# Kernel optimization log

Measured on AMD Instinct MI355X. Metric: run time of the kernel, lower is better.

Reference implementation:

```python
import jax, jax.numpy as jnp
import numpy as np

B, N, M = 262144, 8, 4  # batch, state dim, measurement dim


def _tril_square(x, n):
    """x: (b, n(n+1)/2) linearized lower-tri elems -> L @ L.T, (b, n, n)."""
    i, j = np.tril_indices(n)
    L = jnp.zeros((x.shape[0], n, n), dtype=x.dtype).at[:, i, j].set(x)
    return jnp.einsum('bik,bjk->bij', L, L)


def setup_inputs() -> dict:
    key = jax.random.key(0)
    ks = jax.random.split(key, 7)
    measurement = jax.random.normal(ks[0], (B, M), dtype=jnp.float32)
    state = jax.random.normal(ks[1], (B, N), dtype=jnp.float32)
    # SPD state covariance: A A^T / n + I
    A = jax.random.normal(ks[2], (B, N, N), dtype=jnp.float32) * 0.3
    state_cov = jnp.einsum('bik,bjk->bij', A, A) / N + jnp.eye(N, dtype=jnp.float32)
    F = jnp.eye(N, dtype=jnp.float32) + 0.1 * jax.random.normal(ks[3], (B, N, N), dtype=jnp.float32)
    H = jax.random.normal(ks[4], (B, M, N), dtype=jnp.float32) * 0.5
    process_noise = jax.random.normal(ks[5], (B, N * (N + 1) // 2), dtype=jnp.float32) * 0.1
    measurement_noise = jax.random.normal(ks[6], (B, M * (M + 1) // 2), dtype=jnp.float32) * 0.3
    return {
        'measurement': measurement, 'state': state, 'state_cov': state_cov,
        'F': F, 'H': H,
        'process_noise': process_noise, 'measurement_noise': measurement_noise,
    }


def reference(measurement, state, state_cov, F, H, process_noise, measurement_noise):
    b, n = state.shape
    m = measurement.shape[1]
    Q = _tril_square(process_noise, n)       # (b, n, n) process noise cov
    R = _tril_square(measurement_noise, m)   # (b, m, m) measurement noise cov

    # Predict
    new_state = jnp.einsum('bij,bj->bi', F, state)
    new_state_cov = jnp.einsum('bij,bjk,blk->bil', F, state_cov, F) + Q

    # Update
    prediction = jnp.einsum('bij,bj->bi', H, new_state)
    res = measurement - prediction
    res_cov = jnp.einsum('bij,bjk,blk->bil', H, new_state_cov, H) + R  # (b, m, m)
    PHt = jnp.einsum('bij,bkj->bik', new_state_cov, H)                 # (b, n, m)
    kgain = jnp.matmul(PHt, jnp.linalg.inv(res_cov))                   # (b, n, m)

    upd_state = new_state + jnp.einsum('bij,bj->bi', kgain, res)
    I = jnp.eye(n, dtype=state.dtype)
    upd_cov = jnp.matmul(I - jnp.matmul(kgain, H), new_state_cov)
    return prediction, upd_state, upd_cov
```

## Files before the change

### kernel.cpp

```cpp
#include <hip/hip_runtime.h>

#define DEVINL __device__ __forceinline__

#define TIX(i, j) ((i) * ((i) + 1) / 2 + (j))
#define SYM(arr, i, j) ((i) >= (j) ? arr[TIX(i, j)] : arr[TIX(j, i)])

DEVINL void inv4(const float* m, float* inv) {
    float s0 = m[0] * m[5] - m[1] * m[4];
    float s1 = m[0] * m[6] - m[2] * m[4];
    float s2 = m[0] * m[7] - m[3] * m[4];
    float s3 = m[1] * m[6] - m[2] * m[5];
    float s4 = m[1] * m[7] - m[3] * m[5];
    float s5 = m[2] * m[7] - m[3] * m[6];
    float c5 = m[10] * m[15] - m[11] * m[14];
    float c4 = m[9] * m[15] - m[11] * m[13];
    float c3 = m[9] * m[14] - m[10] * m[13];
    float c2 = m[8] * m[15] - m[11] * m[12];
    float c1 = m[8] * m[14] - m[10] * m[12];
    float c0 = m[8] * m[13] - m[9] * m[12];
    float det = s0 * c5 - s1 * c4 + s2 * c3 + s3 * c2 - s4 * c1 + s5 * c0;
    float id = 1.0f / det;
    inv[0]  = ( m[5] * c5 - m[6] * c4 + m[7] * c3) * id;
    inv[1]  = (-m[1] * c5 + m[2] * c4 - m[3] * c3) * id;
    inv[2]  = ( m[13] * s5 - m[14] * s4 + m[15] * s3) * id;
    inv[3]  = (-m[9] * s5 + m[10] * s4 - m[11] * s3) * id;
    inv[4]  = (-m[4] * c5 + m[6] * c2 - m[7] * c1) * id;
    inv[5]  = ( m[0] * c5 - m[2] * c2 + m[3] * c1) * id;
    inv[6]  = (-m[12] * s5 + m[14] * s2 - m[15] * s1) * id;
    inv[7]  = ( m[8] * s5 - m[10] * s2 + m[11] * s1) * id;
    inv[8]  = ( m[4] * c4 - m[5] * c2 + m[7] * c0) * id;
    inv[9]  = (-m[0] * c4 + m[1] * c2 - m[3] * c0) * id;
    inv[10] = ( m[12] * s4 - m[13] * s2 + m[15] * s0) * id;
    inv[11] = (-m[8] * s4 + m[9] * s2 - m[11] * s0) * id;
    inv[12] = (-m[4] * c3 + m[5] * c1 - m[6] * c0) * id;
    inv[13] = ( m[0] * c3 - m[1] * c1 + m[2] * c0) * id;
    inv[14] = (-m[12] * s3 + m[13] * s1 - m[14] * s0) * id;
    inv[15] = ( m[8] * s3 - m[9] * s1 + m[10] * s0) * id;
}

__global__ __launch_bounds__(256) void ekf_kernel(
    const float* __restrict__ meas,
    const float* __restrict__ state,
    const float* __restrict__ Pin,
    const float* __restrict__ Fin,
    const float* __restrict__ Hin,
    const float* __restrict__ pnin,
    const float* __restrict__ mnin,
    float* __restrict__ out_pred,
    float* __restrict__ out_state,
    float* __restrict__ out_cov,
    int B)
{
    const int b = blockIdx.x * blockDim.x + threadIdx.x;
    if (b >= B) return;

    float Pn[36];
    {
        float Lq[36];
        const float4* p4 = reinterpret_cast<const float4*>(pnin + (size_t)b * 36);
        #pragma unroll
        for (int i = 0; i < 9; ++i) {
            float4 v = p4[i];
            Lq[4 * i] = v.x; Lq[4 * i + 1] = v.y; Lq[4 * i + 2] = v.z; Lq[4 * i + 3] = v.w;
        }
        #pragma unroll
        for (int i = 0; i < 8; ++i)
            #pragma unroll
            for (int j = 0; j <= i; ++j) {
                float acc = 0.f;
                #pragma unroll
                for (int k = 0; k <= j; ++k)
                    acc += Lq[TIX(i, k)] * Lq[TIX(j, k)];
                Pn[TIX(i, j)] = acc;
            }
    }

    float Fm[64];
    {
        const float4* f4 = reinterpret_cast<const float4*>(Fin + (size_t)b * 64);
        #pragma unroll
        for (int i = 0; i < 16; ++i) {
            float4 v = f4[i];
            Fm[4 * i] = v.x; Fm[4 * i + 1] = v.y; Fm[4 * i + 2] = v.z; Fm[4 * i + 3] = v.w;
        }
    }
    float Ps[36];
    {
        const float4* p4 = reinterpret_cast<const float4*>(Pin + (size_t)b * 64);
        #pragma unroll
        for (int i = 0; i < 16; ++i) {
            float4 v = p4[i];
            const int row = i / 2, c0 = (i % 2) * 4;
            if (c0 + 0 <= row) Ps[TIX(row, c0 + 0)] = v.x;
            if (c0 + 1 <= row) Ps[TIX(row, c0 + 1)] = v.y;
            if (c0 + 2 <= row) Ps[TIX(row, c0 + 2)] = v.z;
            if (c0 + 3 <= row) Ps[TIX(row, c0 + 3)] = v.w;
        }
    }
    float s[8];
    {
        const float4* s4 = reinterpret_cast<const float4*>(state + (size_t)b * 8);
        float4 a = s4[0], c = s4[1];
        s[0] = a.x; s[1] = a.y; s[2] = a.z; s[3] = a.w;
        s[4] = c.x; s[5] = c.y; s[6] = c.z; s[7] = c.w;
    }

    float ns[8];
    #pragma unroll
    for (int i = 0; i < 8; ++i) {
        float acc = 0.f;
        #pragma unroll
        for (int j = 0; j < 8; ++j) acc += Fm[i * 8 + j] * s[j];
        ns[i] = acc;
    }

    {
        float T[64];
        #pragma unroll
        for (int i = 0; i < 8; ++i)
            #pragma unroll
            for (int k = 0; k < 8; ++k) {
                float acc = 0.f;
                #pragma unroll
                for (int j = 0; j < 8; ++j) acc += Fm[i * 8 + j] * SYM(Ps, j, k);
                T[i * 8 + k] = acc;
            }
        #pragma unroll
        for (int i = 0; i < 8; ++i)
            #pragma unroll
            for (int l = 0; l <= i; ++l) {
                float acc = Pn[TIX(i, l)];
                #pragma unroll
                for (int k = 0; k < 8; ++k) acc += T[i * 8 + k] * Fm[l * 8 + k];
                Pn[TIX(i, l)] = acc;
            }
    }

    float Hm[32];
    {
        const float4* h4 = reinterpret_cast<const float4*>(Hin + (size_t)b * 32);
        #pragma unroll
        for (int i = 0; i < 8; ++i) {
            float4 v = h4[i];
            Hm[4 * i] = v.x; Hm[4 * i + 1] = v.y; Hm[4 * i + 2] = v.z; Hm[4 * i + 3] = v.w;
        }
    }
    float Rs[10];
    {
        float Lr[10];
        const float2* m2 = reinterpret_cast<const float2*>(mnin + (size_t)b * 10);
        #pragma unroll
        for (int i = 0; i < 5; ++i) {
            float2 v = m2[i];
            Lr[2 * i] = v.x; Lr[2 * i + 1] = v.y;
        }
        #pragma unroll
        for (int i = 0; i < 4; ++i)
            #pragma unroll
            for (int j = 0; j <= i; ++j) {
                float acc = 0.f;
                #pragma unroll
                for (int k = 0; k <= j; ++k)
                    acc += Lr[TIX(i, k)] * Lr[TIX(j, k)];
                Rs[TIX(i, j)] = acc;
            }
    }

    float pred[4], res[4];
    {
        float4 z = *reinterpret_cast<const float4*>(meas + (size_t)b * 4);
        const float zz[4] = {z.x, z.y, z.z, z.w};
        #pragma unroll
        for (int i = 0; i < 4; ++i) {
            float acc = 0.f;
            #pragma unroll
            for (int j = 0; j < 8; ++j) acc += Hm[i * 8 + j] * ns[j];
            pred[i] = acc;
            res[i] = zz[i] - acc;
        }
    }

    float HP[32];
    #pragma unroll
    for (int i = 0; i < 4; ++i)
        #pragma unroll
        for (int k = 0; k < 8; ++k) {
            float acc = 0.f;
            #pragma unroll
            for (int j = 0; j < 8; ++j) acc += Hm[i * 8 + j] * SYM(Pn, j, k);
            HP[i * 8 + k] = acc;
        }

    float Si[16];
    {
        float Sf[16];
        #pragma unroll
        for (int i = 0; i < 4; ++i)
            #pragma unroll
            for (int l = 0; l < 4; ++l) {
                float acc = SYM(Rs, i, l);
                #pragma unroll
                for (int k = 0; k < 8; ++k) acc += HP[i * 8 + k] * Hm[l * 8 + k];
                Sf[i * 4 + l] = acc;
            }
        inv4(Sf, Si);
    }

    float K[32];
    #pragma unroll
    for (int i = 0; i < 8; ++i)
        #pragma unroll
        for (int j = 0; j < 4; ++j) {
            float acc = 0.f;
            #pragma unroll
            for (int k = 0; k < 4; ++k) acc += HP[k * 8 + i] * Si[k * 4 + j];
            K[i * 4 + j] = acc;
        }

    float* op = out_pred + (size_t)b * 4;
    *reinterpret_cast<float4*>(op) = make_float4(pred[0], pred[1], pred[2], pred[3]);

    float us[8];
    #pragma unroll
    for (int i = 0; i < 8; ++i) {
        float acc = ns[i];
        #pragma unroll
        for (int j = 0; j < 4; ++j) acc += K[i * 4 + j] * res[j];
        us[i] = acc;
    }
    float* osp = out_state + (size_t)b * 8;
    *reinterpret_cast<float4*>(osp + 0) = make_float4(us[0], us[1], us[2], us[3]);
    *reinterpret_cast<float4*>(osp + 4) = make_float4(us[4], us[5], us[6], us[7]);

    float* ocp = out_cov + (size_t)b * 64;
    #pragma unroll
    for (int i = 0; i < 8; ++i) {
        float Arow[8];
        #pragma unroll
        for (int j = 0; j < 8; ++j) {
            float acc = (i == j) ? 1.f : 0.f;
            #pragma unroll
            for (int k = 0; k < 4; ++k) acc -= K[i * 4 + k] * Hm[k * 8 + j];
            Arow[j] = acc;
        }
        float orow[8];
        #pragma unroll
        for (int j = 0; j < 8; ++j) {
            float acc = 0.f;
            #pragma unroll
            for (int k = 0; k < 8; ++k) acc += Arow[k] * SYM(Pn, k, j);
            orow[j] = acc;
        }
        *reinterpret_cast<float4*>(ocp + i * 8 + 0) = make_float4(orow[0], orow[1], orow[2], orow[3]);
        *reinterpret_cast<float4*>(ocp + i * 8 + 4) = make_float4(orow[4], orow[5], orow[6], orow[7]);
    }
}

extern "C" void kernel_launch(void* const* d_in, const int* in_sizes, int n_in,
                              void* d_out, int out_size, void* d_ws, size_t ws_size,
                              hipStream_t stream) {
    const float* meas  = (const float*)d_in[0];
    const float* state = (const float*)d_in[1];
    const float* Pin   = (const float*)d_in[2];
    const float* Fin   = (const float*)d_in[3];
    const float* Hin   = (const float*)d_in[4];
    const float* pn    = (const float*)d_in[5];
    const float* mn    = (const float*)d_in[6];

    const int B = in_sizes[1] / 8;

    float* out = (float*)d_out;
    float* out_pred  = out;
    float* out_state = out + (size_t)B * 4;
    float* out_cov   = out + (size_t)B * 12;

    dim3 block(256);
    dim3 grid((B + 255) / 256);
    ekf_kernel<<<grid, block, 0, stream>>>(meas, state, Pin, Fin, Hin, pn, mn,
                                           out_pred, out_state, out_cov, B);
}
```

Before: 271.6 us.

## Stage per-batch loads and stores through padded shared memory for coalescing

Each block now cooperatively loads the per-element inputs (process noise, state, covariance, F, H, measurement noise) into a padded shared buffer with contiguous float4 accesses, then each thread reads its own rows from LDS. The covariance and state outputs are written back the same way. This replaces strided per-thread global float4 accesses (64-256 byte stride) with coalesced ones. It also restructures F·P·F^T into column-wise products, avoiding the 64-entry temporary, and adds a minimum-occupancy launch bound. The cost is many block-wide barriers, about 36 KB of shared memory per block, and extra register pressure under the occupancy hint.

```diff
diff --git a/kernel.cpp b/kernel.cpp
--- a/kernel.cpp
+++ b/kernel.cpp
@@ -38,7 +38,7 @@
     inv[15] = ( m[8] * s3 - m[9] * s1 + m[10] * s0) * id;
 }
 
-__global__ __launch_bounds__(256) void ekf_kernel(
+__global__ __launch_bounds__(256, 3) void ekf_kernel(
     const float* __restrict__ meas,
     const float* __restrict__ state,
     const float* __restrict__ Pin,
@@ -51,17 +51,28 @@
     float* __restrict__ out_cov,
     int B)
 {
-    const int b = blockIdx.x * blockDim.x + threadIdx.x;
-    if (b >= B) return;
-
+    const int t  = threadIdx.x;
+    const int bb = blockIdx.x * 256;
+    const int nb = min(256, B - bb);
+    const int b  = bb + t;
+    const bool act = (t < nb);
+
+    __shared__ float4 buf[2304];
+
+    {
+        const float4* g = reinterpret_cast<const float4*>(pnin) + (size_t)bb * 9;
+        const int lim = nb * 9;
+        #pragma unroll
+        for (int i = 0; i < 9; ++i) { int f = i * 256 + t; if (f < lim) buf[f] = g[f]; }
+    }
+    __syncthreads();
     float Pn[36];
-    {
+    if (act) {
         float Lq[36];
-        const float4* p4 = reinterpret_cast<const float4*>(pnin + (size_t)b * 36);
-        #pragma unroll
-        for (int i = 0; i < 9; ++i) {
-            float4 v = p4[i];
-            Lq[4 * i] = v.x; Lq[4 * i + 1] = v.y; Lq[4 * i + 2] = v.z; Lq[4 * i + 3] = v.w;
+        #pragma unroll
+        for (int q = 0; q < 9; ++q) {
+            float4 v = buf[t * 9 + q];
+            Lq[4 * q] = v.x; Lq[4 * q + 1] = v.y; Lq[4 * q + 2] = v.z; Lq[4 * q + 3] = v.w;
         }
         #pragma unroll
         for (int i = 0; i < 8; ++i)
@@ -74,85 +85,145 @@
                 Pn[TIX(i, j)] = acc;
             }
     }
-
-    float Fm[64];
-    {
-        const float4* f4 = reinterpret_cast<const float4*>(Fin + (size_t)b * 64);
-        #pragma unroll
-        for (int i = 0; i < 16; ++i) {
-            float4 v = f4[i];
-            Fm[4 * i] = v.x; Fm[4 * i + 1] = v.y; Fm[4 * i + 2] = v.z; Fm[4 * i + 3] = v.w;
-        }
-    }
-    float Ps[36];
-    {
-        const float4* p4 = reinterpret_cast<const float4*>(Pin + (size_t)b * 64);
-        #pragma unroll
-        for (int i = 0; i < 16; ++i) {
-            float4 v = p4[i];
-            const int row = i / 2, c0 = (i % 2) * 4;
-            if (c0 + 0 <= row) Ps[TIX(row, c0 + 0)] = v.x;
-            if (c0 + 1 <= row) Ps[TIX(row, c0 + 1)] = v.y;
-            if (c0 + 2 <= row) Ps[TIX(row, c0 + 2)] = v.z;
-            if (c0 + 3 <= row) Ps[TIX(row, c0 + 3)] = v.w;
-        }
-    }
+    __syncthreads();
+
+    {
+        const float4* g = reinterpret_cast<const float4*>(state) + (size_t)bb * 2;
+        const int lim = nb * 2;
+        #pragma unroll
+        for (int i = 0; i < 2; ++i) {
+            int f = i * 256 + t;
+            if (f < lim) buf[(f >> 1) * 3 + (f & 1)] = g[f];
+        }
+    }
+    __syncthreads();
     float s[8];
-    {
-        const float4* s4 = reinterpret_cast<const float4*>(state + (size_t)b * 8);
-        float4 a = s4[0], c = s4[1];
+    if (act) {
+        float4 a = buf[t * 3 + 0], c = buf[t * 3 + 1];
         s[0] = a.x; s[1] = a.y; s[2] = a.z; s[3] = a.w;
         s[4] = c.x; s[5] = c.y; s[6] = c.z; s[7] = c.w;
     }
+    __syncthreads();
+
+    float Ps[36];
+    #pragma unroll
+    for (int h = 0; h < 2; ++h) {
+        {
+            const float4* g = reinterpret_cast<const float4*>(Pin) + (size_t)bb * 16;
+            #pragma unroll
+            for (int i = 0; i < 8; ++i) {
+                int fl = i * 256 + t;
+                int bq = fl >> 3, q = fl & 7;
+                if (bq < nb) buf[bq * 9 + q] = g[bq * 16 + 8 * h + q];
+            }
+        }
+        __syncthreads();
+        if (act) {
+            #pragma unroll
+            for (int q = 0; q < 8; ++q) {
+                float4 v = buf[t * 9 + q];
+                const int row = 4 * h + (q >> 1), c0 = 4 * (q & 1);
+                if (c0 + 0 <= row) Ps[TIX(row, c0 + 0)] = v.x;
+                if (c0 + 1 <= row) Ps[TIX(row, c0 + 1)] = v.y;
+                if (c0 + 2 <= row) Ps[TIX(row, c0 + 2)] = v.z;
+                if (c0 + 3 <= row) Ps[TIX(row, c0 + 3)] = v.w;
+            }
+        }
+        __syncthreads();
+    }
+
+    float Fm[64];
+    #pragma unroll
+    for (int h = 0; h < 2; ++h) {
+        {
+            const float4* g = reinterpret_cast<const float4*>(Fin) + (size_t)bb * 16;
+            #pragma unroll
+            for (int i = 0; i < 8; ++i) {
+                int fl = i * 256 + t;
+                int bq = fl >> 3, q = fl & 7;
+                if (bq < nb) buf[bq * 9 + q] = g[bq * 16 + 8 * h + q];
+            }
+        }
+        __syncthreads();
+        if (act) {
+            #pragma unroll
+            for (int q = 0; q < 8; ++q) {
+                float4 v = buf[t * 9 + q];
+                Fm[32 * h + 4 * q + 0] = v.x;
+                Fm[32 * h + 4 * q + 1] = v.y;
+                Fm[32 * h + 4 * q + 2] = v.z;
+                Fm[32 * h + 4 * q + 3] = v.w;
+            }
+        }
+        __syncthreads();
+    }
 
     float ns[8];
-    #pragma unroll
-    for (int i = 0; i < 8; ++i) {
-        float acc = 0.f;
-        #pragma unroll
-        for (int j = 0; j < 8; ++j) acc += Fm[i * 8 + j] * s[j];
-        ns[i] = acc;
-    }
-
-    {
-        float T[64];
-        #pragma unroll
-        for (int i = 0; i < 8; ++i)
-            #pragma unroll
-            for (int k = 0; k < 8; ++k) {
-                float acc = 0.f;
-                #pragma unroll
-                for (int j = 0; j < 8; ++j) acc += Fm[i * 8 + j] * SYM(Ps, j, k);
-                T[i * 8 + k] = acc;
-            }
-        #pragma unroll
-        for (int i = 0; i < 8; ++i)
-            #pragma unroll
-            for (int l = 0; l <= i; ++l) {
+    if (act) {
+        #pragma unroll
+        for (int i = 0; i < 8; ++i) {
+            float acc = 0.f;
+            #pragma unroll
+            for (int j = 0; j < 8; ++j) acc += Fm[i * 8 + j] * s[j];
+            ns[i] = acc;
+        }
+        #pragma unroll
+        for (int l = 0; l < 8; ++l) {
+            float gcol[8];
+            #pragma unroll
+            for (int j = 0; j < 8; ++j) {
+                float acc = 0.f;
+                #pragma unroll
+                for (int k = 0; k < 8; ++k) acc += SYM(Ps, j, k) * Fm[l * 8 + k];
+                gcol[j] = acc;
+            }
+            #pragma unroll
+            for (int i = l; i < 8; ++i) {
                 float acc = Pn[TIX(i, l)];
                 #pragma unroll
-                for (int k = 0; k < 8; ++k) acc += T[i * 8 + k] * Fm[l * 8 + k];
+                for (int j = 0; j < 8; ++j) acc += Fm[i * 8 + j] * gcol[j];
                 Pn[TIX(i, l)] = acc;
             }
+        }
     }
 
     float Hm[32];
     {
-        const float4* h4 = reinterpret_cast<const float4*>(Hin + (size_t)b * 32);
+        const float4* g = reinterpret_cast<const float4*>(Hin) + (size_t)bb * 8;
+        const int lim = nb * 8;
         #pragma unroll
         for (int i = 0; i < 8; ++i) {
-            float4 v = h4[i];
-            Hm[4 * i] = v.x; Hm[4 * i + 1] = v.y; Hm[4 * i + 2] = v.z; Hm[4 * i + 3] = v.w;
-        }
-    }
+            int fl = i * 256 + t;
+            if (fl < lim) buf[(fl >> 3) * 9 + (fl & 7)] = g[fl];
+        }
+    }
+    __syncthreads();
+    if (act) {
+        #pragma unroll
+        for (int q = 0; q < 8; ++q) {
+            float4 v = buf[t * 9 + q];
+            Hm[4 * q + 0] = v.x; Hm[4 * q + 1] = v.y;
+            Hm[4 * q + 2] = v.z; Hm[4 * q + 3] = v.w;
+        }
+    }
+    __syncthreads();
+
     float Rs[10];
     {
+        const float2* g = reinterpret_cast<const float2*>(mnin) + (size_t)bb * 5;
+        float2* buf2 = reinterpret_cast<float2*>(buf);
+        const int lim = nb * 5;
+        #pragma unroll
+        for (int i = 0; i < 5; ++i) { int f = i * 256 + t; if (f < lim) buf2[f] = g[f]; }
+    }
+    __syncthreads();
+    if (act) {
+        const float2* buf2 = reinterpret_cast<const float2*>(buf);
         float Lr[10];
-        const float2* m2 = reinterpret_cast<const float2*>(mnin + (size_t)b * 10);
-        #pragma unroll
-        for (int i = 0; i < 5; ++i) {
-            float2 v = m2[i];
-            Lr[2 * i] = v.x; Lr[2 * i + 1] = v.y;
+        #pragma unroll
+        for (int p = 0; p < 5; ++p) {
+            float2 v = buf2[t * 5 + p];
+            Lr[2 * p] = v.x; Lr[2 * p + 1] = v.y;
         }
         #pragma unroll
         for (int i = 0; i < 4; ++i)
@@ -165,10 +236,11 @@
                 Rs[TIX(i, j)] = acc;
             }
     }
-
-    float pred[4], res[4];
-    {
-        float4 z = *reinterpret_cast<const float4*>(meas + (size_t)b * 4);
+    __syncthreads();
+
+    float pred[4], res[4], HP[32], Si[16], K[32], us[8];
+    if (act) {
+        float4 z = *(reinterpret_cast<const float4*>(meas) + b);
         const float zz[4] = {z.x, z.y, z.z, z.w};
         #pragma unroll
         for (int i = 0; i < 4; ++i) {
@@ -178,21 +250,17 @@
             pred[i] = acc;
             res[i] = zz[i] - acc;
         }
-    }
-
-    float HP[32];
-    #pragma unroll
-    for (int i = 0; i < 4; ++i)
-        #pragma unroll
-        for (int k = 0; k < 8; ++k) {
-            float acc = 0.f;
-            #pragma unroll
-            for (int j = 0; j < 8; ++j) acc += Hm[i * 8 + j] * SYM(Pn, j, k);
-            HP[i * 8 + k] = acc;
-        }
-
-    float Si[16];
-    {
+
+        #pragma unroll
+        for (int i = 0; i < 4; ++i)
+            #pragma unroll
+            for (int k = 0; k < 8; ++k) {
+                float acc = 0.f;
+                #pragma unroll
+                for (int j = 0; j < 8; ++j) acc += Hm[i * 8 + j] * SYM(Pn, j, k);
+                HP[i * 8 + k] = acc;
+            }
+
         float Sf[16];
         #pragma unroll
         for (int i = 0; i < 4; ++i)
@@ -204,55 +272,83 @@
                 Sf[i * 4 + l] = acc;
             }
         inv4(Sf, Si);
-    }
-
-    float K[32];
+
+        #pragma unroll
+        for (int i = 0; i < 8; ++i)
+            #pragma unroll
+            for (int j = 0; j < 4; ++j) {
+                float acc = 0.f;
+                #pragma unroll
+                for (int k = 0; k < 4; ++k) acc += HP[k * 8 + i] * Si[k * 4 + j];
+                K[i * 4 + j] = acc;
+            }
+
+        *(reinterpret_cast<float4*>(out_pred) + b) =
+            make_float4(pred[0], pred[1], pred[2], pred[3]);
+
+        #pragma unroll
+        for (int i = 0; i < 8; ++i) {
+            float acc = ns[i];
+            #pragma unroll
+            for (int j = 0; j < 4; ++j) acc += K[i * 4 + j] * res[j];
+            us[i] = acc;
+        }
+    }
+
+    __syncthreads();
+    if (act) {
+        buf[t * 3 + 0] = make_float4(us[0], us[1], us[2], us[3]);
+        buf[t * 3 + 1] = make_float4(us[4], us[5], us[6], us[7]);
+    }
+    __syncthreads();
+    {
+        float4* g = reinterpret_cast<float4*>(out_state) + (size_t)bb * 2;
+        const int lim = nb * 2;
+        #pragma unroll
+        for (int i = 0; i < 2; ++i) {
+            int f = i * 256 + t;
+            if (f < lim) g[f] = buf[(f >> 1) * 3 + (f & 1)];
+        }
+    }
+    __syncthreads();
+
     #pragma unroll
-    for (int i = 0; i < 8; ++i)
-        #pragma unroll
-        for (int j = 0; j < 4; ++j) {
-            float acc = 0.f;
-            #pragma unroll
-            for (int k = 0; k < 4; ++k) acc += HP[k * 8 + i] * Si[k * 4 + j];
-            K[i * 4 + j] = acc;
-        }
-
-    float* op = out_pred + (size_t)b * 4;
-    *reinterpret_cast<float4*>(op) = make_float4(pred[0], pred[1], pred[2], pred[3]);
-
-    float us[8];
-    #pragma unroll
-    for (int i = 0; i < 8; ++i) {
-        float acc = ns[i];
-        #pragma unroll
-        for (int j = 0; j < 4; ++j) acc += K[i * 4 + j] * res[j];
-        us[i] = acc;
-    }
-    float* osp = out_state + (size_t)b * 8;
-    *reinterpret_cast<float4*>(osp + 0) = make_float4(us[0], us[1], us[2], us[3]);
-    *reinterpret_cast<float4*>(osp + 4) = make_float4(us[4], us[5], us[6], us[7]);
-
-    float* ocp = out_cov + (size_t)b * 64;
-    #pragma unroll
-    for (int i = 0; i < 8; ++i) {
-        float Arow[8];
-        #pragma unroll
-        for (int j = 0; j < 8; ++j) {
-            float acc = (i == j) ? 1.f : 0.f;
-            #pragma unroll
-            for (int k = 0; k < 4; ++k) acc -= K[i * 4 + k] * Hm[k * 8 + j];
-            Arow[j] = acc;
-        }
-        float orow[8];
-        #pragma unroll
-        for (int j = 0; j < 8; ++j) {
-            float acc = 0.f;
-            #pragma unroll
-            for (int k = 0; k < 8; ++k) acc += Arow[k] * SYM(Pn, k, j);
-            orow[j] = acc;
-        }
-        *reinterpret_cast<float4*>(ocp + i * 8 + 0) = make_float4(orow[0], orow[1], orow[2], orow[3]);
-        *reinterpret_cast<float4*>(ocp + i * 8 + 4) = make_float4(orow[4], orow[5], orow[6], orow[7]);
+    for (int h = 0; h < 2; ++h) {
+        if (act) {
+            #pragma unroll
+            for (int r = 0; r < 4; ++r) {
+                const int i = 4 * h + r;
+                float Arow[8];
+                #pragma unroll
+                for (int j = 0; j < 8; ++j) {
+                    float acc = (i == j) ? 1.f : 0.f;
+                    #pragma unroll
+                    for (int k = 0; k < 4; ++k) acc -= K[i * 4 + k] * Hm[k * 8 + j];
+                    Arow[j] = acc;
+                }
+                float orow[8];
+                #pragma unroll
+                for (int j = 0; j < 8; ++j) {
+                    float acc = 0.f;
+                    #pragma unroll
+                    for (int k = 0; k < 8; ++k) acc += Arow[k] * SYM(Pn, k, j);
+                    orow[j] = acc;
+                }
+                buf[t * 9 + 2 * r + 0] = make_float4(orow[0], orow[1], orow[2], orow[3]);
+                buf[t * 9 + 2 * r + 1] = make_float4(orow[4], orow[5], orow[6], orow[7]);
+            }
+        }
+        __syncthreads();
+        {
+            float4* g = reinterpret_cast<float4*>(out_cov) + (size_t)bb * 16;
+            #pragma unroll
+            for (int i = 0; i < 8; ++i) {
+                int fl = i * 256 + t;
+                int bq = fl >> 3, q = fl & 7;
+                if (bq < nb) g[bq * 16 + 8 * h + q] = buf[bq * 9 + q];
+            }
+        }
+        __syncthreads();
     }
 }
 
```

New measurement: 342.1 us. 1.26x slower.

## Split each Kalman filter batch across 8 lanes with shuffle-based row math

Applied to the files above, without the earlier changes.

Instead of one thread per batch element holding full 8x8 matrices in registers, each batch element is now handled by 8 lanes, one per state row. Matrix products and reductions are exchanged via width-8 shuffles. The covariance update is rewritten as P - (HP)^T S^-1 (HP), dropping the explicit Kalman gain and the I-KH product. The aim is to cut register pressure, raise occupancy and coalesce loads and stores. In exchange, the 4x4 inverse is computed redundantly in every lane, and the bounds check is dropped, so B*8 must be a multiple of 256.

```diff
diff --git a/kernel.cpp b/kernel.cpp
--- a/kernel.cpp
+++ b/kernel.cpp
@@ -1,9 +1,7 @@
 #include <hip/hip_runtime.h>
 
 #define DEVINL __device__ __forceinline__
-
 #define TIX(i, j) ((i) * ((i) + 1) / 2 + (j))
-#define SYM(arr, i, j) ((i) >= (j) ? arr[TIX(i, j)] : arr[TIX(j, i)])
 
 DEVINL void inv4(const float* m, float* inv) {
     float s0 = m[0] * m[5] - m[1] * m[4];
@@ -48,212 +46,153 @@
     const float* __restrict__ mnin,
     float* __restrict__ out_pred,
     float* __restrict__ out_state,
-    float* __restrict__ out_cov,
-    int B)
+    float* __restrict__ out_cov)
 {
-    const int b = blockIdx.x * blockDim.x + threadIdx.x;
-    if (b >= B) return;
-
-    float Pn[36];
+    const int gt = blockIdx.x * 256 + threadIdx.x;
+    const int b  = gt >> 3;
+    const int r  = gt & 7;
+
+    float fr[8], pr[8];
     {
-        float Lq[36];
-        const float4* p4 = reinterpret_cast<const float4*>(pnin + (size_t)b * 36);
-        #pragma unroll
-        for (int i = 0; i < 9; ++i) {
-            float4 v = p4[i];
-            Lq[4 * i] = v.x; Lq[4 * i + 1] = v.y; Lq[4 * i + 2] = v.z; Lq[4 * i + 3] = v.w;
-        }
-        #pragma unroll
-        for (int i = 0; i < 8; ++i)
+        const float4* gf = reinterpret_cast<const float4*>(Fin + (size_t)b * 64 + r * 8);
+        float4 a = gf[0], c = gf[1];
+        fr[0]=a.x; fr[1]=a.y; fr[2]=a.z; fr[3]=a.w;
+        fr[4]=c.x; fr[5]=c.y; fr[6]=c.z; fr[7]=c.w;
+        const float4* gp = reinterpret_cast<const float4*>(Pin + (size_t)b * 64 + r * 8);
+        float4 d = gp[0], e = gp[1];
+        pr[0]=d.x; pr[1]=d.y; pr[2]=d.z; pr[3]=d.w;
+        pr[4]=e.x; pr[5]=e.y; pr[6]=e.z; pr[7]=e.w;
+    }
+    float lq[8];
+    {
+        const float* lp = pnin + (size_t)b * 36 + ((r * (r + 1)) >> 1);
+        #pragma unroll
+        for (int k = 0; k < 8; ++k) { float v = lp[k]; lq[k] = (k <= r) ? v : 0.f; }
+    }
+    float hc[4];
+    #pragma unroll
+    for (int a = 0; a < 4; ++a) hc[a] = Hin[(size_t)b * 32 + a * 8 + r];
+    float sc = state[(size_t)b * 8 + r];
+    float4 z = *reinterpret_cast<const float4*>(meas + (size_t)b * 4);
+
+    float ns = 0.f;
+    #pragma unroll
+    for (int j = 0; j < 8; ++j) ns += fr[j] * __shfl(sc, j, 8);
+
+    float g[8];
+    #pragma unroll
+    for (int l = 0; l < 8; ++l) {
+        float acc = 0.f;
+        #pragma unroll
+        for (int k = 0; k < 8; ++k) acc += pr[k] * __shfl(fr[k], l, 8);
+        g[l] = acc;
+    }
+
+    float pn_[8] = {0, 0, 0, 0, 0, 0, 0, 0};
+    #pragma unroll
+    for (int j = 0; j < 8; ++j) {
+        const float frj = fr[j];
+        #pragma unroll
+        for (int l = 0; l < 8; ++l) pn_[l] += frj * __shfl(g[l], j, 8);
+    }
+
+    #pragma unroll
+    for (int l = 0; l < 8; ++l) {
+        float acc = 0.f;
+        #pragma unroll
+        for (int k = 0; k <= l; ++k) acc += lq[k] * __shfl(lq[k], l, 8);
+        pn_[l] += acc;
+    }
+
+    float pd[4];
+    #pragma unroll
+    for (int a = 0; a < 4; ++a) pd[a] = hc[a] * ns;
+    #pragma unroll
+    for (int a = 0; a < 4; ++a) {
+        pd[a] += __shfl_xor(pd[a], 1, 8);
+        pd[a] += __shfl_xor(pd[a], 2, 8);
+        pd[a] += __shfl_xor(pd[a], 4, 8);
+    }
+    float res[4] = { z.x - pd[0], z.y - pd[1], z.z - pd[2], z.w - pd[3] };
+    if (r < 4) {
+        float pv = pd[0];
+        pv = (r == 1) ? pd[1] : pv;
+        pv = (r == 2) ? pd[2] : pv;
+        pv = (r == 3) ? pd[3] : pv;
+        out_pred[(size_t)b * 4 + r] = pv;
+    }
+
+    float hp[4] = {0, 0, 0, 0};
+    #pragma unroll
+    for (int j = 0; j < 8; ++j) {
+        const float pj = pn_[j];
+        #pragma unroll
+        for (int a = 0; a < 4; ++a) hp[a] += pj * __shfl(hc[a], j, 8);
+    }
+
+    float S[16];
+    #pragma unroll
+    for (int a = 0; a < 4; ++a)
+        #pragma unroll
+        for (int c = 0; c < 4; ++c) S[a * 4 + c] = hp[a] * hc[c];
+    #pragma unroll
+    for (int e = 0; e < 16; ++e) {
+        S[e] += __shfl_xor(S[e], 1, 8);
+        S[e] += __shfl_xor(S[e], 2, 8);
+        S[e] += __shfl_xor(S[e], 4, 8);
+    }
+    {
+        float lr[10];
+        const float2* g2 = reinterpret_cast<const float2*>(mnin + (size_t)b * 10);
+        #pragma unroll
+        for (int i = 0; i < 5; ++i) { float2 v = g2[i]; lr[2 * i] = v.x; lr[2 * i + 1] = v.y; }
+        #pragma unroll
+        for (int a = 0; a < 4; ++a)
             #pragma unroll
-            for (int j = 0; j <= i; ++j) {
+            for (int c = 0; c <= a; ++c) {
                 float acc = 0.f;
                 #pragma unroll
-                for (int k = 0; k <= j; ++k)
-                    acc += Lq[TIX(i, k)] * Lq[TIX(j, k)];
-                Pn[TIX(i, j)] = acc;
+                for (int k = 0; k <= c; ++k) acc += lr[TIX(a, k)] * lr[TIX(c, k)];
+                S[a * 4 + c] += acc;
+                if (a != c) S[c * 4 + a] += acc;
             }
     }
-
-    float Fm[64];
-    {
-        const float4* f4 = reinterpret_cast<const float4*>(Fin + (size_t)b * 64);
-        #pragma unroll
-        for (int i = 0; i < 16; ++i) {
-            float4 v = f4[i];
-            Fm[4 * i] = v.x; Fm[4 * i + 1] = v.y; Fm[4 * i + 2] = v.z; Fm[4 * i + 3] = v.w;
-        }
-    }
-    float Ps[36];
-    {
-        const float4* p4 = reinterpret_cast<const float4*>(Pin + (size_t)b * 64);
-        #pragma unroll
-        for (int i = 0; i < 16; ++i) {
-            float4 v = p4[i];
-            const int row = i / 2, c0 = (i % 2) * 4;
-            if (c0 + 0 <= row) Ps[TIX(row, c0 + 0)] = v.x;
-            if (c0 + 1 <= row) Ps[TIX(row, c0 + 1)] = v.y;
-            if (c0 + 2 <= row) Ps[TIX(row, c0 + 2)] = v.z;
-            if (c0 + 3 <= row) Ps[TIX(row, c0 + 3)] = v.w;
-        }
-    }
-    float s[8];
-    {
-        const float4* s4 = reinterpret_cast<const float4*>(state + (size_t)b * 8);
-        float4 a = s4[0], c = s4[1];
-        s[0] = a.x; s[1] = a.y; s[2] = a.z; s[3] = a.w;
-        s[4] = c.x; s[5] = c.y; s[6] = c.z; s[7] = c.w;
-    }
-
-    float ns[8];
-    #pragma unroll
-    for (int i = 0; i < 8; ++i) {
-        float acc = 0.f;
-        #pragma unroll
-        for (int j = 0; j < 8; ++j) acc += Fm[i * 8 + j] * s[j];
-        ns[i] = acc;
-    }
-
-    {
-        float T[64];
-        #pragma unroll
-        for (int i = 0; i < 8; ++i)
-            #pragma unroll
-            for (int k = 0; k < 8; ++k) {
-                float acc = 0.f;
-                #pragma unroll
-                for (int j = 0; j < 8; ++j) acc += Fm[i * 8 + j] * SYM(Ps, j, k);
-                T[i * 8 + k] = acc;
-            }
-        #pragma unroll
-        for (int i = 0; i < 8; ++i)
-            #pragma unroll
-            for (int l = 0; l <= i; ++l) {
-                float acc = Pn[TIX(i, l)];
-                #pragma unroll
-                for (int k = 0; k < 8; ++k) acc += T[i * 8 + k] * Fm[l * 8 + k];
-                Pn[TIX(i, l)] = acc;
-            }
-    }
-
-    float Hm[32];
-    {
-        const float4* h4 = reinterpret_cast<const float4*>(Hin + (size_t)b * 32);
-        #pragma unroll
-        for (int i = 0; i < 8; ++i) {
-            float4 v = h4[i];
-            Hm[4 * i] = v.x; Hm[4 * i + 1] = v.y; Hm[4 * i + 2] = v.z; Hm[4 * i + 3] = v.w;
-        }
-    }
-    float Rs[10];
-    {
-        float Lr[10];
-        const float2* m2 = reinterpret_cast<const float2*>(mnin + (size_t)b * 10);
-        #pragma unroll
-        for (int i = 0; i < 5; ++i) {
-            float2 v = m2[i];
-            Lr[2 * i] = v.x; Lr[2 * i + 1] = v.y;
-        }
-        #pragma unroll
-        for (int i = 0; i < 4; ++i)
-            #pragma unroll
-            for (int j = 0; j <= i; ++j) {
-                float acc = 0.f;
-                #pragma unroll
-                for (int k = 0; k <= j; ++k)
-                    acc += Lr[TIX(i, k)] * Lr[TIX(j, k)];
-                Rs[TIX(i, j)] = acc;
-            }
-    }
-
-    float pred[4], res[4];
-    {
-        float4 z = *reinterpret_cast<const float4*>(meas + (size_t)b * 4);
-        const float zz[4] = {z.x, z.y, z.z, z.w};
-        #pragma unroll
-        for (int i = 0; i < 4; ++i) {
-            float acc = 0.f;
-            #pragma unroll
-            for (int j = 0; j < 8; ++j) acc += Hm[i * 8 + j] * ns[j];
-            pred[i] = acc;
-            res[i] = zz[i] - acc;
-        }
-    }
-
-    float HP[32];
-    #pragma unroll
-    for (int i = 0; i < 4; ++i)
-        #pragma unroll
-        for (int k = 0; k < 8; ++k) {
-            float acc = 0.f;
-            #pragma unroll
-            for (int j = 0; j < 8; ++j) acc += Hm[i * 8 + j] * SYM(Pn, j, k);
-            HP[i * 8 + k] = acc;
-        }
-
     float Si[16];
-    {
-        float Sf[16];
-        #pragma unroll
-        for (int i = 0; i < 4; ++i)
-            #pragma unroll
-            for (int l = 0; l < 4; ++l) {
-                float acc = SYM(Rs, i, l);
-                #pragma unroll
-                for (int k = 0; k < 8; ++k) acc += HP[i * 8 + k] * Hm[l * 8 + k];
-                Sf[i * 4 + l] = acc;
-            }
-        inv4(Sf, Si);
-    }
-
-    float K[32];
-    #pragma unroll
-    for (int i = 0; i < 8; ++i)
-        #pragma unroll
-        for (int j = 0; j < 4; ++j) {
-            float acc = 0.f;
-            #pragma unroll
-            for (int k = 0; k < 4; ++k) acc += HP[k * 8 + i] * Si[k * 4 + j];
-            K[i * 4 + j] = acc;
-        }
-
-    float* op = out_pred + (size_t)b * 4;
-    *reinterpret_cast<float4*>(op) = make_float4(pred[0], pred[1], pred[2], pred[3]);
-
-    float us[8];
-    #pragma unroll
-    for (int i = 0; i < 8; ++i) {
-        float acc = ns[i];
-        #pragma unroll
-        for (int j = 0; j < 4; ++j) acc += K[i * 4 + j] * res[j];
-        us[i] = acc;
-    }
-    float* osp = out_state + (size_t)b * 8;
-    *reinterpret_cast<float4*>(osp + 0) = make_float4(us[0], us[1], us[2], us[3]);
-    *reinterpret_cast<float4*>(osp + 4) = make_float4(us[4], us[5], us[6], us[7]);
-
-    float* ocp = out_cov + (size_t)b * 64;
-    #pragma unroll
-    for (int i = 0; i < 8; ++i) {
-        float Arow[8];
-        #pragma unroll
-        for (int j = 0; j < 8; ++j) {
-            float acc = (i == j) ? 1.f : 0.f;
-            #pragma unroll
-            for (int k = 0; k < 4; ++k) acc -= K[i * 4 + k] * Hm[k * 8 + j];
-            Arow[j] = acc;
-        }
-        float orow[8];
-        #pragma unroll
-        for (int j = 0; j < 8; ++j) {
-            float acc = 0.f;
-            #pragma unroll
-            for (int k = 0; k < 8; ++k) acc += Arow[k] * SYM(Pn, k, j);
-            orow[j] = acc;
-        }
-        *reinterpret_cast<float4*>(ocp + i * 8 + 0) = make_float4(orow[0], orow[1], orow[2], orow[3]);
-        *reinterpret_cast<float4*>(ocp + i * 8 + 4) = make_float4(orow[4], orow[5], orow[6], orow[7]);
-    }
+    inv4(S, Si);
+
+    float w[4];
+    #pragma unroll
+    for (int a = 0; a < 4; ++a) {
+        float acc = 0.f;
+        #pragma unroll
+        for (int c = 0; c < 4; ++c) acc += Si[a * 4 + c] * res[c];
+        w[a] = acc;
+    }
+    float us = ns;
+    #pragma unroll
+    for (int a = 0; a < 4; ++a) us += hp[a] * w[a];
+    out_state[(size_t)b * 8 + r] = us;
+
+    float m_[4];
+    #pragma unroll
+    for (int a = 0; a < 4; ++a) {
+        float acc = 0.f;
+        #pragma unroll
+        for (int c = 0; c < 4; ++c) acc += Si[a * 4 + c] * hp[c];
+        m_[a] = acc;
+    }
+
+    float cv[8];
+    #pragma unroll
+    for (int l = 0; l < 8; ++l) {
+        float acc = pn_[l];
+        #pragma unroll
+        for (int a = 0; a < 4; ++a) acc -= hp[a] * __shfl(m_[a], l, 8);
+        cv[l] = acc;
+    }
+    float4* oc = reinterpret_cast<float4*>(out_cov + (size_t)b * 64 + r * 8);
+    oc[0] = make_float4(cv[0], cv[1], cv[2], cv[3]);
+    oc[1] = make_float4(cv[4], cv[5], cv[6], cv[7]);
 }
 
 extern "C" void kernel_launch(void* const* d_in, const int* in_sizes, int n_in,
@@ -275,7 +214,7 @@
     float* out_cov   = out + (size_t)B * 12;
 
     dim3 block(256);
-    dim3 grid((B + 255) / 256);
+    dim3 grid((B * 8) / 256);
     ekf_kernel<<<grid, block, 0, stream>>>(meas, state, Pin, Fin, Hin, pn, mn,
-                                           out_pred, out_state, out_cov, B);
+                                           out_pred, out_state, out_cov);
 }
```

New measurement: 270.6 us. About the same (-0.3%).
